# Optimization experiments

Measured on AMD Instinct MI355X. Metric: run time of the kernel, lower is better.

The kernel has to match this reference:

```python
import jax, jax.numpy as jnp
import numpy as np

G = 8          # groups
PATCH = 4      # encoder patch conv kernel/stride
MD = 4         # correlation max displacement -> (2*MD+1)^2 = 81 neighbours
BNEPS = 1e-5
LNEPS = 1e-5

# finite-difference gradient kernel (assumed: forward differences on a C-grid)
GRAD_K = jnp.array([[[[0., 0., 0.], [0., -1., 1.], [0., 0., 0.]]],
                    [[[0., 0., 0.], [0., -1., 0.], [0., 1., 0.]]]], dtype=jnp.float32)

def _vort_kernel():
    # assumed 6x6 Biot-Savart-like vorticity->velocity kernel (CalculusOperators not in source)
    c = 2.5
    ys, xs = np.mgrid[0:6, 0:6].astype(np.float32)
    r2 = (ys - c) ** 2 + (xs - c) ** 2
    u = -(ys - c) / (2.0 * np.pi * r2)
    v = (xs - c) / (2.0 * np.pi * r2)
    return jnp.asarray(np.stack([u, v])[:, None])  # [2,1,6,6]
VORT_K = _vort_kernel()

def conv2d(x, w, pad, stride=1):
    return jax.lax.conv_general_dilated(x, w, (stride, stride), [(pad, pad), (pad, pad)],
                                        dimension_numbers=('NCHW', 'OIHW', 'NCHW'))

def bn(x, g, b):
    # inference-mode BatchNorm with running_mean=0, running_var=1
    return x * (g / jnp.sqrt(1.0 + BNEPS))[None, :, None, None] + b[None, :, None, None]

def up2x(x):
    def lerp_axis(x, axis):
        n = x.shape[axis]
        c = jnp.arange(2 * n, dtype=x.dtype) * (n - 1) / (2 * n - 1)
        i0 = jnp.floor(c).astype(jnp.int32)
        i1 = jnp.minimum(i0 + 1, n - 1)
        w = c - i0.astype(x.dtype)
        a0 = jnp.take(x, i0, axis=axis)
        a1 = jnp.take(x, i1, axis=axis)
        shp = [1] * x.ndim; shp[axis] = 2 * n
        w = w.reshape(shp)
        return a0 * (1 - w) + a1 * w
    return lerp_axis(lerp_axis(x, 2), 3)

def double_conv_up(x, w1, g1, b1, w2, g2, b2):
    x = jax.nn.relu(bn(conv2d(up2x(x), w1, 1), g1, b1))
    return jax.nn.relu(bn(conv2d(up2x(x), w2, 1), g2, b2))

@jax.checkpoint
def correlation(f1, f2):
    # PWC-Net style FunctionCorrelation: mean over channels of f1 * shifted f2, 81 shifts
    N, C, H, W = f1.shape
    f2p = jnp.pad(f2, ((0, 0), (0, 0), (MD, MD), (MD, MD)))
    outs = [jnp.mean(f1 * f2p[:, :, dy:dy + H, dx:dx + W], axis=1)
            for dy in range(2 * MD + 1) for dx in range(2 * MD + 1)]
    return jnp.stack(outs, axis=1)  # [N, 81, H, W]

def cgrid_to_motion(u, v, shape):
    mu = (u[:, :, 1:-1, 1:] + u[:, :, 1:-1, :-1]) * 0.5
    mv = (v[:, :, 1:, 1:-1] + v[:, :, :-1, 1:-1]) * 0.5
    m = jnp.concatenate([mu, mv], axis=1)
    h, w = shape
    up = (m.shape[2] - h) // 2
    left = (m.shape[3] - w) // 2
    return m[:, :, up:up + h, left:left + w]

def calc_phi_velocity(phi, shape):
    vel = conv2d(phi, GRAD_K, 1)
    return cgrid_to_motion(vel[:, 0:1, :, :-1], vel[:, 1:2, :-1, :], shape)

def calc_vort_velocity(stream, shape):
    s = stream[:, :, :-1, :-1]
    vel = conv2d(s, VORT_K, 5)  # full-padding conv == conv_transpose of flipped kernel
    return cgrid_to_motion(vel[:, 0:1, 2:-2, 2:-3], vel[:, 1:2, 2:-3, 2:-2], shape)

def bilinear_sample(f, px, py):
    # f [N,C,H,W]; px,py [N,H,W] absolute coords, border clamp
    H, W = f.shape[-2], f.shape[-1]
    px = jnp.clip(px, 0.0, W - 1.0)
    py = jnp.clip(py, 0.0, H - 1.0)
    x0 = jnp.floor(px); y0 = jnp.floor(py)
    wx = (px - x0)[:, None]; wy = (py - y0)[:, None]
    x0i = x0.astype(jnp.int32); y0i = y0.astype(jnp.int32)
    x1i = jnp.minimum(x0i + 1, W - 1); y1i = jnp.minimum(y0i + 1, H - 1)
    gat = jax.vmap(lambda fi, yi, xi: fi[:, yi, xi])
    v00 = gat(f, y0i, x0i); v01 = gat(f, y0i, x1i)
    v10 = gat(f, y1i, x0i); v11 = gat(f, y1i, x1i)
    return (v00 * (1 - wx) + v01 * wx) * (1 - wy) + (v10 * (1 - wx) + v11 * wx) * wy

def warp(f, vel, sign):
    N, _, H, W = f.shape
    ys, xs = jnp.meshgrid(jnp.arange(H, dtype=f.dtype), jnp.arange(W, dtype=f.dtype), indexing='ij')
    return bilinear_sample(f, xs[None] - sign * vel[:, 0], ys[None] - sign * vel[:, 1])

def bfecc_warp(f, vel):
    f1 = warp(f, vel, 1.0)
    fb = warp(f1, vel, -1.0)
    return warp(f + 0.5 * (f - fb), vel, 1.0)

def _forward(prev, next, texture, mask, boundary,
             enc_w, enc_b,
             phi_w1, phi_g1, phi_b1, phi_w2, phi_g2, phi_b2, phi_ow, phi_ob,
             vor_w1, vor_g1, vor_b1, vor_w2, vor_g2, vor_b2, vor_ow, vor_ob,
             phi_weight, vorticity_weight,
             ln_g, ln_b, fc1_w, fc1_b, fc2_w, fc2_b):
    B, C, H, W = prev.shape
    shape = texture.shape[-2:]
    pm = (prev * mask[:, None]).reshape(B * G, C // G, H, W)
    pb = (prev * boundary[:, None]).reshape(B * G, C // G, H, W)
    nm = (next * mask[:, None]).reshape(B * G, C // G, H, W)
    enc = lambda x: conv2d(x, enc_w, 0, PATCH) + enc_b[None, :, None, None]
    f_nm = enc(nm)
    corr = jnp.concatenate([correlation(enc(pm), f_nm), correlation(enc(pb), f_nm)], axis=1)
    phi = (conv2d(double_conv_up(corr, phi_w1, phi_g1, phi_b1, phi_w2, phi_g2, phi_b2), phi_ow, 0)
           + phi_ob[None, :, None, None]) * phi_weight
    vort = (conv2d(double_conv_up(corr, vor_w1, vor_g1, vor_b1, vor_w2, vor_g2, vor_b2), vor_ow, 0)
            + vor_ob[None, :, None, None]) * vorticity_weight * H
    helm = jnp.concatenate([phi, vort], axis=1)  # [B*G, 2, H, W]
    vel_phi = calc_phi_velocity(helm[:, 0:1], shape)
    vel_vort = calc_vort_velocity(helm[:, 1:2], shape)
    vel = vel_phi + vel_vort
    Bt, Ct, Ht, Wt = texture.shape
    tex = texture.reshape(B * G, Ct // G, Ht, Wt)
    pred = bfecc_warp(tex, vel).reshape(B, Ct, Ht, Wt)
    xp = jnp.transpose(pred, (0, 2, 3, 1))  # [B,H,W,C]
    mu = jnp.mean(xp, -1, keepdims=True)
    var = jnp.var(xp, -1, keepdims=True)
    y = (xp - mu) / jnp.sqrt(var + LNEPS) * ln_g + ln_b
    y = jax.nn.gelu(y @ fc1_w.T + fc1_b, approximate=False)
    y = y @ fc2_w.T + fc2_b
    return pred + jnp.transpose(y, (0, 3, 1, 2))

def setup_inputs():
    ks = jax.random.split(jax.random.key(0), 20)
    B, C, H, W = 4, 64, 260, 260
    Ht, Wt = 258, 258
    D = 128           # correlation_dim
    cg = C // G       # 8 channels per group
    ed = 8            # encoder_dim // groups = 64 // 8
    n = lambda i, shp, s=1.0: jax.random.normal(ks[i], shp, jnp.float32) * s
    return {
        'prev': n(0, (B, C, H, W)), 'next': n(1, (B, C, H, W)),
        'texture': n(2, (B, C, Ht, Wt)),
        'mask': jax.random.uniform(ks[3], (B, H, W), jnp.float32),
        'boundary': jax.random.uniform(ks[4], (B, H, W), jnp.float32),
        'enc_w': n(5, (D, cg, PATCH, PATCH), 0.05), 'enc_b': n(6, (D,), 0.02),
        'phi_w1': n(7, (ed, 162, 3, 3), 0.05), 'phi_g1': jnp.ones(ed), 'phi_b1': jnp.zeros(ed),
        'phi_w2': n(8, (ed, ed, 3, 3), 0.05), 'phi_g2': jnp.ones(ed), 'phi_b2': jnp.zeros(ed),
        'phi_ow': n(9, (1, ed, 1, 1), 0.05), 'phi_ob': n(10, (1,), 0.02),
        'vor_w1': n(11, (ed, 162, 3, 3), 0.05), 'vor_g1': jnp.ones(ed), 'vor_b1': jnp.zeros(ed),
        'vor_w2': n(12, (ed, ed, 3, 3), 0.05), 'vor_g2': jnp.ones(ed), 'vor_b2': jnp.zeros(ed),
        'vor_ow': n(13, (1, ed, 1, 1), 0.05), 'vor_ob': n(14, (1,), 0.02),
        'phi_weight': jnp.array([0.5], jnp.float32),
        'vorticity_weight': jnp.array([0.005], jnp.float32),
        'ln_g': jnp.ones(C), 'ln_b': jnp.zeros(C),
        'fc1_w': n(15, (C, C), 0.05), 'fc1_b': n(16, (C,), 0.02),
        'fc2_w': n(17, (C, C), 0.05), 'fc2_b': n(18, (C,), 0.02),
    }

def reference(prev, next, texture, mask, boundary,
              enc_w, enc_b,
              phi_w1, phi_g1, phi_b1, phi_w2, phi_g2, phi_b2, phi_ow, phi_ob,
              vor_w1, vor_g1, vor_b1, vor_w2, vor_g2, vor_b2, vor_ow, vor_ob,
              phi_weight, vorticity_weight,
              ln_g, ln_b, fc1_w, fc1_b, fc2_w, fc2_b):
    return _forward(prev, next, texture, mask, boundary,
                    enc_w, enc_b,
                    phi_w1, phi_g1, phi_b1, phi_w2, phi_g2, phi_b2, phi_ow, phi_ob,
                    vor_w1, vor_g1, vor_b1, vor_w2, vor_g2, vor_b2, vor_ow, vor_ob,
                    phi_weight, vorticity_weight,
                    ln_g, ln_b, fc1_w, fc1_b, fc2_w, fc2_b)
```

## Files before the change

kernel.cpp:

```cpp
#include <hip/hip_runtime.h>
#include <math.h>


#define NIMG 32
#define HW 260
#define HWT 258
#define EG 65
#define EGP (EG*EG)
#define DENC 128
#define PIX_T (HWT*HWT)
#define PIX_H (HW*HW)

__global__ void k_wt(const float* __restrict__ w, float* __restrict__ wt) {
    int e = blockIdx.x * 256 + threadIdx.x;
    if (e < 128 * 128) {
        int d = e >> 7, i = e & 127;
        wt[i * 128 + d] = w[e];
    }
}

__global__ __launch_bounds__(128) void k_enc(
    const float* __restrict__ src,
    const float* __restrict__ mul,
    const float* __restrict__ wt,
    const float* __restrict__ bias,
    float* __restrict__ out)
{
    int xt = blockIdx.x;
    int yo = blockIdx.y;
    int n  = blockIdx.z;
    int bi = n >> 3, g = n & 7;
    int xo0 = xt * 16;
    __shared__ __align__(16) float patch[2048];
    int tid = threadIdx.x;
    const float* sbase = src + (size_t)(bi * 64 + g * 8) * PIX_H;
    const float* mbase = mul + (size_t)bi * PIX_H;
    int row0 = yo * 4, col0 = xo0 * 4;
    for (int e = tid; e < 2048; e += 128) {
        int c = e >> 8, r = (e >> 6) & 3, col = e & 63;
        int gc = col0 + col;
        float v = 0.f;
        if (gc < HW) {
            int off = (row0 + r) * HW + gc;
            v = sbase[(size_t)c * PIX_H + off] * mbase[off];
        }
        patch[e] = v;
    }
    __syncthreads();
    int d = tid;
    float acc[16];
    float bv = bias[d];
#pragma unroll
    for (int p = 0; p < 16; ++p) acc[p] = bv;
    const float4* p4 = (const float4*)patch;
    for (int j = 0; j < 32; ++j) {
        float w0 = wt[(j * 4 + 0) * 128 + d];
        float w1 = wt[(j * 4 + 1) * 128 + d];
        float w2 = wt[(j * 4 + 2) * 128 + d];
        float w3 = wt[(j * 4 + 3) * 128 + d];
#pragma unroll
        for (int p = 0; p < 16; ++p) {
            float4 v = p4[j * 16 + p];
            acc[p] += w0 * v.x + w1 * v.y + w2 * v.z + w3 * v.w;
        }
    }
    size_t ob = ((size_t)(n * EG + yo) * EG + xo0) * 128 + d;
#pragma unroll
    for (int p = 0; p < 16; ++p)
        if (xo0 + p < EG) out[ob + (size_t)p * 128] = acc[p];
}

__global__ __launch_bounds__(128) void k_corr(
    const float* __restrict__ f1,
    const float* __restrict__ f2,
    float* __restrict__ corr,
    int obase)
{
    int bx = blockIdx.x;
    int dy = bx >> 1, xt = bx & 1;
    int y  = blockIdx.y;
    int n  = blockIdx.z;
    int xs = xt ? 33 : 0;
    int nx = xt ? 32 : 33;
    __shared__ __align__(16) float s1[33 * 132];
    __shared__ __align__(16) float s2[41 * 132];
    int tid = threadIdx.x;
    const float4* g1 = (const float4*)(f1 + ((size_t)(n * EG + y) * EG + xs) * 128);
    float4* s1v = (float4*)s1;
    for (int e = tid; e < nx * 32; e += 128) {
        int xl = e >> 5, c4 = e & 31;
        s1v[xl * 33 + c4] = g1[xl * 32 + c4];
    }
    int y2 = y + dy - 4;
    bool yok = (y2 >= 0 && y2 < EG);
    const float4* g2 = (const float4*)(f2 + (yok ? ((size_t)(n * EG + y2) * EG) * 128 : 0));
    float4* s2v = (float4*)s2;
    for (int e = tid; e < 41 * 32; e += 128) {
        int xl = e >> 5, c4 = e & 31;
        int xg = xs - 4 + xl;
        float4 v = make_float4(0.f, 0.f, 0.f, 0.f);
        if (yok && xg >= 0 && xg < EG) v = g2[xg * 32 + c4];
        s2v[xl * 33 + c4] = v;
    }
    __syncthreads();
    int nact = nx * 3;
    if (tid < nact) {
        int q, xl;
        if (xt) { q = tid >> 5; xl = tid & 31; }
        else    { q = tid / 33; xl = tid - q * 33; }
        int dx0 = q * 3;
        float4 a0 = make_float4(0,0,0,0), a1 = a0, a2 = a0;
        const float4* r1 = (const float4*)s1 + xl * 33;
        const float4* r2 = (const float4*)s2 + (xl + dx0) * 33;
#pragma unroll 8
        for (int i = 0; i < 32; ++i) {
            float4 a = r1[i];
            float4 b0 = r2[i], b1 = r2[33 + i], b2 = r2[66 + i];
            a0.x += a.x * b0.x; a0.y += a.y * b0.y; a0.z += a.z * b0.z; a0.w += a.w * b0.w;
            a1.x += a.x * b1.x; a1.y += a.y * b1.y; a1.z += a.z * b1.z; a1.w += a.w * b1.w;
            a2.x += a.x * b2.x; a2.y += a.y * b2.y; a2.z += a.z * b2.z; a2.w += a.w * b2.w;
        }
        float s[3];
        s[0] = (a0.x + a0.y + a0.z + a0.w) * (1.0f / 128.0f);
        s[1] = (a1.x + a1.y + a1.z + a1.w) * (1.0f / 128.0f);
        s[2] = (a2.x + a2.y + a2.z + a2.w) * (1.0f / 128.0f);
#pragma unroll
        for (int m = 0; m < 3; ++m) {
            int o = obase + dy * 9 + dx0 + m;
            corr[(size_t)(n * 162 + o) * EGP + y * EG + xs + xl] = s[m];
        }
    }
}

__global__ __launch_bounds__(256) void k_conv1(
    const float* __restrict__ corr,
    const float* __restrict__ w_phi,
    const float* __restrict__ w_vor,
    const float* __restrict__ g_phi, const float* __restrict__ b_phi,
    const float* __restrict__ g_vor, const float* __restrict__ b_vor,
    float* __restrict__ h1)
{
    int yp = blockIdx.x;
    int n  = blockIdx.y;
    int y0 = yp * 4;
    __shared__ float upc[6 * 6 * 132];
    __shared__ float wch[16 * 6 * 9];
    __shared__ float s_xw[132];
    __shared__ int   s_xi0[132];
    __shared__ int   s_xi1[132];
    __shared__ float s_yw[6];
    __shared__ int   s_yj0[6];
    __shared__ int   s_yj1[6];
    __shared__ int   s_yv[6];
    int tid = threadIdx.x;
    if (tid < 132) {
        int xu = tid - 1;
        if (xu >= 0 && xu <= 129) {
            float cx = (float)(xu * 64) / 129.0f;
            int i0 = (int)cx;
            int i1 = i0 + 1; if (i1 > 64) i1 = 64;
            s_xw[tid] = cx - (float)i0;
            s_xi0[tid] = i0;
            s_xi1[tid] = i1;
        } else { s_xi0[tid] = -1; s_xi1[tid] = 0; s_xw[tid] = 0.f; }
    }
    if (tid >= 132 && tid < 138) {
        int r = tid - 132;
        int yy = y0 - 1 + r;
        if (yy >= 0 && yy <= 129) {
            float cy = (float)(yy * 64) / 129.0f;
            int i0 = (int)cy;
            int i1 = i0 + 1; if (i1 > 64) i1 = 64;
            s_yw[r] = cy - (float)i0;
            s_yj0[r] = i0;
            s_yj1[r] = i1;
            s_yv[r] = 1;
        } else { s_yw[r] = 0.f; s_yj0[r] = 0; s_yj1[r] = 0; s_yv[r] = 0; }
    }
    int og = tid / 26, xg = tid - og * 26;
    int x0 = xg * 5;
    bool act = (og < 8);
    float acc[2][4][5] = {};
    for (int cc = 0; cc < 27; ++cc) {
        int cb = cc * 6;
        __syncthreads();
        for (int e = tid; e < 4752; e += 256) {
            int r = e / 792, rem = e - r * 792, ci = rem / 132, xx = rem - ci * 132;
            float val = 0.f;
            int xi0 = s_xi0[xx];
            if (s_yv[r] && xi0 >= 0) {
                const float* cp = corr + (size_t)(n * 162 + cb + ci) * EGP;
                int J0 = s_yj0[r] * 65, J1 = s_yj1[r] * 65;
                int xi1 = s_xi1[xx];
                float wxv = s_xw[xx];
                float a0 = __ldg(cp + J0 + xi0), a1 = __ldg(cp + J0 + xi1);
                float b0 = __ldg(cp + J1 + xi0), b1 = __ldg(cp + J1 + xi1);
                float tp = a0 + wxv * (a1 - a0);
                float bt = b0 + wxv * (b1 - b0);
                val = tp + s_yw[r] * (bt - tp);
            }
            upc[e] = val;
        }
        for (int e = tid; e < 864; e += 256) {
            int oc = e / 54, rem = e - oc * 54, ci = rem / 9, k = rem - ci * 9;
            int t2 = oc >> 3, o = oc & 7;
            wch[e] = (t2 ? w_vor : w_phi)[(o * 162 + cb + ci) * 9 + k];
        }
        __syncthreads();
        if (act) {
            for (int ci = 0; ci < 6; ++ci) {
                float wr[2][9];
#pragma unroll
                for (int p = 0; p < 2; ++p)
#pragma unroll
                    for (int k = 0; k < 9; ++k)
                        wr[p][k] = wch[((og + 8 * p) * 6 + ci) * 9 + k];
#pragma unroll
                for (int r = 0; r < 6; ++r) {
                    float u7[7];
                    const float* up = &upc[(r * 6 + ci) * 132 + x0];
#pragma unroll
                    for (int m = 0; m < 7; ++m) u7[m] = up[m];
#pragma unroll
                    for (int ky = 0; ky < 3; ++ky) {
                        int yi = r - ky;
                        if (yi < 0 || yi > 3) continue;
#pragma unroll
                        for (int p = 0; p < 2; ++p)
#pragma unroll
                            for (int kx = 0; kx < 3; ++kx) {
                                float w = wr[p][ky * 3 + kx];
#pragma unroll
                                for (int xi = 0; xi < 5; ++xi)
                                    acc[p][yi][xi] += w * u7[xi + kx];
                            }
                    }
                }
            }
        }
    }
    if (act) {
        const float bnsc = 1.0f / sqrtf(1.0f + 1e-5f);
#pragma unroll
        for (int p = 0; p < 2; ++p) {
            float gsc = (p ? g_vor[og] : g_phi[og]) * bnsc;
            float bia = (p ? b_vor[og] : b_phi[og]);
            size_t pb = (size_t)((p * 32 + n) * 8 + og) * 16900;
#pragma unroll
            for (int yi = 0; yi < 4; ++yi) {
                int row = y0 + yi;
                if (row < 130) {
#pragma unroll
                    for (int xi = 0; xi < 5; ++xi) {
                        float v = acc[p][yi][xi] * gsc + bia;
                        h1[pb + (size_t)row * 130 + (x0 + xi)] = fmaxf(v, 0.f);
                    }
                }
            }
        }
    }
}

__global__ __launch_bounds__(256) void k_conv2(
    const float* __restrict__ h1,
    const float* __restrict__ w_phi2, const float* __restrict__ w_vor2,
    const float* __restrict__ g_phi2, const float* __restrict__ b_phi2,
    const float* __restrict__ g_vor2, const float* __restrict__ b_vor2,
    const float* __restrict__ ow_phi, const float* __restrict__ ob_phi,
    const float* __restrict__ ow_vor, const float* __restrict__ ob_vor,
    const float* __restrict__ phi_weight, const float* __restrict__ vort_weight,
    float* __restrict__ helm)
{
    int y = blockIdx.x, n = blockIdx.y;
    __shared__ float hraw[8320];
    __shared__ float wch[1152];
    __shared__ float bns[16], bnb[16], owv[16], obv[2], wm[2];
    int tid = threadIdx.x;
    int ylo = y - 1; if (ylo < 0) ylo = 0;
    int R0 = (int)((float)(ylo * 129) / 259.0f);
    for (int e = tid; e < 8320; e += 256) {
        int t2 = e / 4160, rem = e - t2 * 4160;
        int j = rem / 1040, rem2 = rem - j * 1040;
        int ci = rem2 / 130, xx = rem2 - ci * 130;
        int R = R0 + j; if (R > 129) R = 129;
        hraw[e] = h1[(size_t)((t2 * 32 + n) * 8 + ci) * 16900 + R * 130 + xx];
    }
    for (int e = tid; e < 1152; e += 256) {
        int t2 = e / 576, rem = e - t2 * 576;
        int o = rem / 72, rem2 = rem - o * 72;
        int ci = rem2 / 9, k = rem2 - ci * 9;
        wch[e] = (t2 ? w_vor2 : w_phi2)[(o * 8 + ci) * 9 + k];
    }
    if (tid < 16) {
        int t2 = tid >> 3, o = tid & 7;
        bns[tid] = (t2 ? g_vor2[o] : g_phi2[o]) * (1.0f / sqrtf(1.0f + 1e-5f));
        bnb[tid] = (t2 ? b_vor2[o] : b_phi2[o]);
        owv[tid] = (t2 ? ow_vor[o] : ow_phi[o]);
    }
    if (tid == 0) {
        obv[0] = ob_phi[0]; obv[1] = ob_vor[0];
        wm[0] = phi_weight[0]; wm[1] = vort_weight[0] * 260.0f;
    }
    __syncthreads();
    for (int x = tid; x < HW; x += 256) {
        float wy[3]; int rj0[3], rj1[3]; bool vy[3];
#pragma unroll
        for (int ky = 0; ky < 3; ++ky) {
            int yy = y - 1 + ky;
            vy[ky] = (yy >= 0 && yy < HW);
            if (vy[ky]) {
                float cy = (float)(yy * 129) / 259.0f;
                int i0 = (int)cy; wy[ky] = cy - (float)i0;
                int i1 = i0 + 1; if (i1 > 129) i1 = 129;
                rj0[ky] = i0 - R0; rj1[ky] = i1 - R0;
            } else { wy[ky] = 0; rj0[ky] = 0; rj1[ky] = 0; }
        }
        float wxv[3]; int c0[3], c1[3]; bool vx[3];
#pragma unroll
        for (int kx = 0; kx < 3; ++kx) {
            int xxp = x - 1 + kx;
            vx[kx] = (xxp >= 0 && xxp < HW);
            if (vx[kx]) {
                float cx = (float)(xxp * 129) / 259.0f;
                int i0 = (int)cx; wxv[kx] = cx - (float)i0;
                int i1 = i0 + 1; if (i1 > 129) i1 = 129;
                c0[kx] = i0; c1[kx] = i1;
            } else { wxv[kx] = 0; c0[kx] = 0; c1[kx] = 0; }
        }
        float res[2];
#pragma unroll
        for (int t2 = 0; t2 < 2; ++t2) {
            float acc[8] = {0,0,0,0,0,0,0,0};
            for (int ci = 0; ci < 8; ++ci) {
#pragma unroll
                for (int ky = 0; ky < 3; ++ky) {
                    if (!vy[ky]) continue;
                    const float* r0p = &hraw[((t2 * 4 + rj0[ky]) * 8 + ci) * 130];
                    const float* r1p = &hraw[((t2 * 4 + rj1[ky]) * 8 + ci) * 130];
                    float u3[3];
#pragma unroll
                    for (int kx = 0; kx < 3; ++kx) {
                        if (vx[kx]) {
                            float tp = r0p[c0[kx]] + wxv[kx] * (r0p[c1[kx]] - r0p[c0[kx]]);
                            float bt = r1p[c0[kx]] + wxv[kx] * (r1p[c1[kx]] - r1p[c0[kx]]);
                            u3[kx] = tp + wy[ky] * (bt - tp);
                        } else u3[kx] = 0.f;
                    }
#pragma unroll
                    for (int o = 0; o < 8; ++o) {
                        const float* wp = &wch[((t2 * 8 + o) * 8 + ci) * 9 + ky * 3];
                        acc[o] += wp[0] * u3[0] + wp[1] * u3[1] + wp[2] * u3[2];
                    }
                }
            }
            float dot = 0.f;
#pragma unroll
            for (int o = 0; o < 8; ++o) {
                float hv = fmaxf(acc[o] * bns[t2 * 8 + o] + bnb[t2 * 8 + o], 0.f);
                dot += owv[t2 * 8 + o] * hv;
            }
            res[t2] = (dot + obv[t2]) * wm[t2];
        }
        helm[(size_t)(n * 2 + 0) * PIX_H + y * HW + x] = res[0];
        helm[(size_t)(n * 2 + 1) * PIX_H + y * HW + x] = res[1];
    }
}

__device__ __forceinline__ float K0f(int a, int b) {
    if (a < 0 || a > 5 || b < 0 || b > 5) return 0.f;
    float fa = (float)a - 2.5f, fb = (float)b - 2.5f;
    float r2 = fa * fa + fb * fb;
    return -fa / (6.28318530717958647692f * r2);
}
__device__ __forceinline__ float K1f(int a, int b) {
    if (a < 0 || a > 5 || b < 0 || b > 5) return 0.f;
    float fa = (float)a - 2.5f, fb = (float)b - 2.5f;
    float r2 = fa * fa + fb * fb;
    return fb / (6.28318530717958647692f * r2);
}

__global__ __launch_bounds__(256) void k_vel(
    const float* __restrict__ helm, float* __restrict__ vel)
{
    int idx = blockIdx.x * 256 + threadIdx.x;
    if (idx >= NIMG * PIX_T) return;
    int n = idx / PIX_T, pix = idx - n * PIX_T;
    int yy = pix / HWT, xx = pix - yy * HWT;
    const float* phi = helm + (size_t)(n * 2) * PIX_H;
    const float* s   = helm + (size_t)(n * 2 + 1) * PIX_H;
    float sv[7][7];
#pragma unroll
    for (int di = 0; di < 7; ++di) {
        int i = yy + di - 3;
#pragma unroll
        for (int dj = 0; dj < 7; ++dj) {
            int j = xx + dj - 3;
            sv[di][dj] = (i >= 0 && i < 259 && j >= 0 && j < 259) ? s[i * HW + j] : 0.f;
        }
    }
    float ax = 0.5f * (phi[(yy + 1) * HW + xx + 2] - phi[(yy + 1) * HW + xx]);
#pragma unroll
    for (int a = 0; a < 6; ++a)
#pragma unroll
        for (int d = 0; d < 7; ++d) {
            float coef = K0f(a, d) + K0f(a, d - 1);
            ax += 0.5f * coef * sv[a + 1][d];
        }
    float ay = 0.5f * (phi[(yy + 2) * HW + xx + 1] - phi[yy * HW + xx + 1]);
#pragma unroll
    for (int d = 0; d < 7; ++d)
#pragma unroll
        for (int b = 0; b < 6; ++b) {
            float coef = K1f(d, b) + K1f(d - 1, b);
            ay += 0.5f * coef * sv[d][b + 1];
        }
    vel[(size_t)(n * 2) * PIX_T + pix]     = ax;
    vel[(size_t)(n * 2 + 1) * PIX_T + pix] = ay;
}

__device__ __forceinline__ float bsample(const float* __restrict__ plane,
                                         float px, float py) {
    px = fminf(fmaxf(px, 0.f), 257.f);
    py = fminf(fmaxf(py, 0.f), 257.f);
    float fx = floorf(px), fy = floorf(py);
    int x0 = (int)fx, y0 = (int)fy;
    float wx = px - fx, wy = py - fy;
    int x1 = x0 + 1; if (x1 > 257) x1 = 257;
    int y1 = y0 + 1; if (y1 > 257) y1 = 257;
    const float* r0 = plane + y0 * HWT;
    const float* r1 = plane + y1 * HWT;
    float v00 = r0[x0], v01 = r0[x1], v10 = r1[x0], v11 = r1[x1];
    float tp = v00 + wx * (v01 - v00);
    float bt = v10 + wx * (v11 - v10);
    return tp + wy * (bt - tp);
}

__global__ __launch_bounds__(256) void k_warp(
    const float* __restrict__ src,
    const float* __restrict__ vel,
    float sign,
    const float* __restrict__ tex,
    int mode,
    float* __restrict__ out)
{
    int idx = blockIdx.x * 256 + threadIdx.x;
    if (idx >= NIMG * 8 * PIX_T) return;
    int plane_i = idx / PIX_T;
    int pix = idx - plane_i * PIX_T;
    int n = plane_i >> 3;
    int y = pix / HWT, x = pix - y * HWT;
    float vx = vel[(size_t)(n * 2) * PIX_T + pix];
    float vy = vel[(size_t)(n * 2 + 1) * PIX_T + pix];
    const float* plane = src + (size_t)plane_i * PIX_T;
    float v = bsample(plane, (float)x - sign * vx, (float)y - sign * vy);
    if (mode) v = 1.5f * tex[idx] - 0.5f * v;
    out[idx] = v;
}

__global__ __launch_bounds__(256, 2) void k_lnmlp(
    float* __restrict__ out,
    const float* __restrict__ lng, const float* __restrict__ lnb,
    const float* __restrict__ w1, const float* __restrict__ b1,
    const float* __restrict__ w2, const float* __restrict__ b2)
{
    int yy = blockIdx.x, b = blockIdx.y;
    __shared__ __align__(16) float sw1[4096];
    __shared__ __align__(16) float sw2t[4096];
    __shared__ float sb1[64], sb2[64], sg[64], sbt[64];
    int tid = threadIdx.x;
    for (int e = tid; e < 4096; e += 256) {
        sw1[e] = w1[e];
        sw2t[(e & 63) * 64 + (e >> 6)] = w2[e];
    }
    if (tid < 64) { sb1[tid] = b1[tid]; sb2[tid] = b2[tid]; sg[tid] = lng[tid]; sbt[tid] = lnb[tid]; }
    __syncthreads();
    float* base = out + (size_t)b * 64 * PIX_T + (size_t)yy * HWT;
    for (int x = tid; x < HWT; x += 256) {
        float sum = 0.f, sumsq = 0.f;
        for (int k = 0; k < 64; ++k) {
            float v = base[(size_t)k * PIX_T + x];
            sum += v; sumsq += v * v;
        }
        float mu = sum * (1.0f / 64.0f);
        float var = sumsq * (1.0f / 64.0f) - mu * mu;
        float inv = 1.0f / sqrtf(var + 1e-5f);
        float xn[64];
#pragma unroll
        for (int k = 0; k < 64; ++k) {
            float v = base[(size_t)k * PIX_T + x];
            xn[k] = (v - mu) * inv * sg[k] + sbt[k];
        }
        float acc2[64];
#pragma unroll
        for (int j2 = 0; j2 < 64; ++j2) acc2[j2] = 0.f;
        for (int j = 0; j < 64; ++j) {
            float t = sb1[j];
            const float4* wrow = (const float4*)&sw1[j * 64];
#pragma unroll
            for (int k4 = 0; k4 < 16; ++k4) {
                float4 w = wrow[k4];
                t += xn[4 * k4] * w.x + xn[4 * k4 + 1] * w.y
                   + xn[4 * k4 + 2] * w.z + xn[4 * k4 + 3] * w.w;
            }
            float hj = 0.5f * t * (1.0f + erff(t * 0.70710678118654752f));
            const float4* w2row = (const float4*)&sw2t[j * 64];
#pragma unroll
            for (int q = 0; q < 16; ++q) {
                float4 w = w2row[q];
                acc2[4 * q]     += hj * w.x;
                acc2[4 * q + 1] += hj * w.y;
                acc2[4 * q + 2] += hj * w.z;
                acc2[4 * q + 3] += hj * w.w;
            }
        }
#pragma unroll
        for (int j2 = 0; j2 < 64; ++j2)
            base[(size_t)j2 * PIX_T + x] += sb2[j2] + acc2[j2];
    }
}

extern "C" void kernel_launch(void* const* d_in, const int* in_sizes, int n_in,
                              void* d_out, int out_size, void* d_ws, size_t ws_size,
                              hipStream_t stream) {
    const float* prev       = (const float*)d_in[0];
    const float* next       = (const float*)d_in[1];
    const float* texture    = (const float*)d_in[2];
    const float* mask       = (const float*)d_in[3];
    const float* boundary   = (const float*)d_in[4];
    const float* enc_w      = (const float*)d_in[5];
    const float* enc_b      = (const float*)d_in[6];
    const float* phi_w1     = (const float*)d_in[7];
    const float* phi_g1     = (const float*)d_in[8];
    const float* phi_b1     = (const float*)d_in[9];
    const float* phi_w2     = (const float*)d_in[10];
    const float* phi_g2     = (const float*)d_in[11];
    const float* phi_b2     = (const float*)d_in[12];
    const float* phi_ow     = (const float*)d_in[13];
    const float* phi_ob     = (const float*)d_in[14];
    const float* vor_w1     = (const float*)d_in[15];
    const float* vor_g1     = (const float*)d_in[16];
    const float* vor_b1     = (const float*)d_in[17];
    const float* vor_w2     = (const float*)d_in[18];
    const float* vor_g2     = (const float*)d_in[19];
    const float* vor_b2     = (const float*)d_in[20];
    const float* vor_ow     = (const float*)d_in[21];
    const float* vor_ob     = (const float*)d_in[22];
    const float* phi_weight = (const float*)d_in[23];
    const float* vor_weight = (const float*)d_in[24];
    const float* ln_g       = (const float*)d_in[25];
    const float* ln_b       = (const float*)d_in[26];
    const float* fc1_w      = (const float*)d_in[27];
    const float* fc1_b      = (const float*)d_in[28];
    const float* fc2_w      = (const float*)d_in[29];
    const float* fc2_b      = (const float*)d_in[30];

    float* ws = (float*)d_ws;
    float* F_NM = ws + 0;
    float* F_A  = ws + 17305600;
    float* CORR = ws + 34611200;
    float* WT   = ws + 56513600;
    float* H1   = ws + 0;
    float* HELM = ws + 17305600;
    float* VEL  = ws + 21632000;
    float* F1B  = ws + 34611200;
    float* F2B  = ws + 0;
    float* OUT  = (float*)d_out;

    k_wt<<<dim3(64), dim3(256), 0, stream>>>(enc_w, WT);

    dim3 encg(5, 65, 32);
    k_enc<<<encg, dim3(128), 0, stream>>>(next, mask, WT, enc_b, F_NM);
    k_enc<<<encg, dim3(128), 0, stream>>>(prev, mask, WT, enc_b, F_A);

    dim3 corrg(18, 65, 32);
    k_corr<<<corrg, dim3(128), 0, stream>>>(F_A, F_NM, CORR, 0);
    k_enc<<<encg, dim3(128), 0, stream>>>(prev, boundary, WT, enc_b, F_A);
    k_corr<<<corrg, dim3(128), 0, stream>>>(F_A, F_NM, CORR, 81);

    k_conv1<<<dim3(33, 32), dim3(256), 0, stream>>>(
        CORR, phi_w1, vor_w1, phi_g1, phi_b1, vor_g1, vor_b1, H1);

    k_conv2<<<dim3(260, 32), dim3(256), 0, stream>>>(
        H1, phi_w2, vor_w2, phi_g2, phi_b2, vor_g2, vor_b2,
        phi_ow, phi_ob, vor_ow, vor_ob, phi_weight, vor_weight, HELM);

    int nv = NIMG * PIX_T;
    k_vel<<<dim3((nv + 255) / 256), dim3(256), 0, stream>>>(HELM, VEL);

    int nw = NIMG * 8 * PIX_T;
    int wb = (nw + 255) / 256;
    k_warp<<<dim3(wb), dim3(256), 0, stream>>>(texture, VEL,  1.0f, texture, 0, F1B);
    k_warp<<<dim3(wb), dim3(256), 0, stream>>>(F1B,     VEL, -1.0f, texture, 1, F2B);
    k_warp<<<dim3(wb), dim3(256), 0, stream>>>(F2B,     VEL,  1.0f, texture, 0, OUT);

    k_lnmlp<<<dim3(258, 4), dim3(256), 0, stream>>>(
        OUT, ln_g, ln_b, fc1_w, fc1_b, fc2_w, fc2_b);
}
```

Baseline: 3.075 ms.

## Split conv1 input channels across grid z with a reduction kernel; halve corr LDS

The first upsample-conv stage now splits its 27 input-channel chunks into three slices along grid z. Each slice writes raw partial sums to a workspace buffer, and a new elementwise kernel sums the three partials and applies BN and ReLU. This triples the block count for a grid that was small relative to the GPU, at the cost of extra partial-sum traffic and one more launch. Separately, the correlation kernel stages channels in two 64-channel halves using float4 shared arrays. This roughly halves its LDS footprint so more blocks can be resident, but adds barriers.

```diff
diff --git a/kernel.cpp b/kernel.cpp
--- a/kernel.cpp
+++ b/kernel.cpp
@@ -7,9 +7,9 @@
 #define HWT 258
 #define EG 65
 #define EGP (EG*EG)
-#define DENC 128
 #define PIX_T (HWT*HWT)
 #define PIX_H (HW*HW)
+#define H1N 8652800
 
 __global__ void k_wt(const float* __restrict__ w, float* __restrict__ wt) {
     int e = blockIdx.x * 256 + threadIdx.x;
@@ -82,44 +82,48 @@
     int n  = blockIdx.z;
     int xs = xt ? 33 : 0;
     int nx = xt ? 32 : 33;
-    __shared__ __align__(16) float s1[33 * 132];
-    __shared__ __align__(16) float s2[41 * 132];
+    __shared__ __align__(16) float4 s1[33 * 17];
+    __shared__ __align__(16) float4 s2[41 * 17];
     int tid = threadIdx.x;
     const float4* g1 = (const float4*)(f1 + ((size_t)(n * EG + y) * EG + xs) * 128);
-    float4* s1v = (float4*)s1;
-    for (int e = tid; e < nx * 32; e += 128) {
-        int xl = e >> 5, c4 = e & 31;
-        s1v[xl * 33 + c4] = g1[xl * 32 + c4];
-    }
     int y2 = y + dy - 4;
     bool yok = (y2 >= 0 && y2 < EG);
     const float4* g2 = (const float4*)(f2 + (yok ? ((size_t)(n * EG + y2) * EG) * 128 : 0));
-    float4* s2v = (float4*)s2;
-    for (int e = tid; e < 41 * 32; e += 128) {
-        int xl = e >> 5, c4 = e & 31;
-        int xg = xs - 4 + xl;
-        float4 v = make_float4(0.f, 0.f, 0.f, 0.f);
-        if (yok && xg >= 0 && xg < EG) v = g2[xg * 32 + c4];
-        s2v[xl * 33 + c4] = v;
-    }
-    __syncthreads();
-    int nact = nx * 3;
-    if (tid < nact) {
-        int q, xl;
-        if (xt) { q = tid >> 5; xl = tid & 31; }
-        else    { q = tid / 33; xl = tid - q * 33; }
-        int dx0 = q * 3;
-        float4 a0 = make_float4(0,0,0,0), a1 = a0, a2 = a0;
-        const float4* r1 = (const float4*)s1 + xl * 33;
-        const float4* r2 = (const float4*)s2 + (xl + dx0) * 33;
+    int q, xl;
+    if (xt) { q = tid >> 5; xl = tid & 31; }
+    else    { q = tid / 33; xl = tid - q * 33; }
+    int dx0 = q * 3;
+    bool act = tid < nx * 3;
+    float4 a0 = make_float4(0,0,0,0), a1 = a0, a2 = a0;
+    for (int half = 0; half < 2; ++half) {
+        int cb = half * 16;
+        __syncthreads();
+        for (int e = tid; e < nx * 16; e += 128) {
+            int r = e >> 4, c4 = e & 15;
+            s1[r * 17 + c4] = g1[r * 32 + cb + c4];
+        }
+        for (int e = tid; e < 41 * 16; e += 128) {
+            int r = e >> 4, c4 = e & 15;
+            int xg = xs - 4 + r;
+            float4 v = make_float4(0.f, 0.f, 0.f, 0.f);
+            if (yok && xg >= 0 && xg < EG) v = g2[xg * 32 + cb + c4];
+            s2[r * 17 + c4] = v;
+        }
+        __syncthreads();
+        if (act) {
+            const float4* r1 = s1 + xl * 17;
+            const float4* r2 = s2 + (xl + dx0) * 17;
 #pragma unroll 8
-        for (int i = 0; i < 32; ++i) {
-            float4 a = r1[i];
-            float4 b0 = r2[i], b1 = r2[33 + i], b2 = r2[66 + i];
-            a0.x += a.x * b0.x; a0.y += a.y * b0.y; a0.z += a.z * b0.z; a0.w += a.w * b0.w;
-            a1.x += a.x * b1.x; a1.y += a.y * b1.y; a1.z += a.z * b1.z; a1.w += a.w * b1.w;
-            a2.x += a.x * b2.x; a2.y += a.y * b2.y; a2.z += a.z * b2.z; a2.w += a.w * b2.w;
-        }
+            for (int i = 0; i < 16; ++i) {
+                float4 a = r1[i];
+                float4 b0 = r2[i], b1 = r2[17 + i], b2 = r2[34 + i];
+                a0.x += a.x * b0.x; a0.y += a.y * b0.y; a0.z += a.z * b0.z; a0.w += a.w * b0.w;
+                a1.x += a.x * b1.x; a1.y += a.y * b1.y; a1.z += a.z * b1.z; a1.w += a.w * b1.w;
+                a2.x += a.x * b2.x; a2.y += a.y * b2.y; a2.z += a.z * b2.z; a2.w += a.w * b2.w;
+            }
+        }
+    }
+    if (act) {
         float s[3];
         s[0] = (a0.x + a0.y + a0.z + a0.w) * (1.0f / 128.0f);
         s[1] = (a1.x + a1.y + a1.z + a1.w) * (1.0f / 128.0f);
@@ -136,12 +140,11 @@
     const float* __restrict__ corr,
     const float* __restrict__ w_phi,
     const float* __restrict__ w_vor,
-    const float* __restrict__ g_phi, const float* __restrict__ b_phi,
-    const float* __restrict__ g_vor, const float* __restrict__ b_vor,
-    float* __restrict__ h1)
+    float* __restrict__ part)
 {
     int yp = blockIdx.x;
     int n  = blockIdx.y;
+    int zp = blockIdx.z;
     int y0 = yp * 4;
     __shared__ float upc[6 * 6 * 132];
     __shared__ float wch[16 * 6 * 9];
@@ -181,7 +184,7 @@
     int x0 = xg * 5;
     bool act = (og < 8);
     float acc[2][4][5] = {};
-    for (int cc = 0; cc < 27; ++cc) {
+    for (int cc = zp * 9; cc < zp * 9 + 9; ++cc) {
         int cb = cc * 6;
         __syncthreads();
         for (int e = tid; e < 4752; e += 256) {
@@ -240,25 +243,47 @@
         }
     }
     if (act) {
-        const float bnsc = 1.0f / sqrtf(1.0f + 1e-5f);
+        float* pbuf = part + (size_t)zp * H1N;
 #pragma unroll
         for (int p = 0; p < 2; ++p) {
-            float gsc = (p ? g_vor[og] : g_phi[og]) * bnsc;
-            float bia = (p ? b_vor[og] : b_phi[og]);
             size_t pb = (size_t)((p * 32 + n) * 8 + og) * 16900;
 #pragma unroll
             for (int yi = 0; yi < 4; ++yi) {
                 int row = y0 + yi;
                 if (row < 130) {
 #pragma unroll
-                    for (int xi = 0; xi < 5; ++xi) {
-                        float v = acc[p][yi][xi] * gsc + bia;
-                        h1[pb + (size_t)row * 130 + (x0 + xi)] = fmaxf(v, 0.f);
-                    }
+                    for (int xi = 0; xi < 5; ++xi)
+                        pbuf[pb + (size_t)row * 130 + (x0 + xi)] = acc[p][yi][xi];
                 }
             }
         }
     }
+}
+
+__global__ __launch_bounds__(256) void k_h1red(
+    const float* __restrict__ part,
+    const float* __restrict__ g_phi, const float* __restrict__ b_phi,
+    const float* __restrict__ g_vor, const float* __restrict__ b_vor,
+    float* __restrict__ h1)
+{
+    int i4 = blockIdx.x * 256 + threadIdx.x;
+    if (i4 >= H1N / 4) return;
+    size_t i = (size_t)i4 * 4;
+    int c2 = (int)(i / 16900);
+    int o = c2 & 7, t2 = c2 >> 8;
+    const float bnsc = 1.0f / sqrtf(1.0f + 1e-5f);
+    float gsc = (t2 ? g_vor[o] : g_phi[o]) * bnsc;
+    float bia = (t2 ? b_vor[o] : b_phi[o]);
+    const float4* p0 = (const float4*)(part);
+    const float4* p1 = (const float4*)(part + H1N);
+    const float4* p2 = (const float4*)(part + 2 * (size_t)H1N);
+    float4 a = p0[i4], b = p1[i4], c = p2[i4];
+    float4 r;
+    r.x = fmaxf((a.x + b.x + c.x) * gsc + bia, 0.f);
+    r.y = fmaxf((a.y + b.y + c.y) * gsc + bia, 0.f);
+    r.z = fmaxf((a.z + b.z + c.z) * gsc + bia, 0.f);
+    r.w = fmaxf((a.w + b.w + c.w) * gsc + bia, 0.f);
+    ((float4*)h1)[i4] = r;
 }
 
 __global__ __launch_bounds__(256) void k_conv2(
@@ -559,7 +584,8 @@
     float* F_A  = ws + 17305600;
     float* CORR = ws + 34611200;
     float* WT   = ws + 56513600;
-    float* H1   = ws + 0;
+    float* PART = ws + 0;
+    float* H1   = ws + 25958400;
     float* HELM = ws + 17305600;
     float* VEL  = ws + 21632000;
     float* F1B  = ws + 34611200;
@@ -577,8 +603,10 @@
     k_enc<<<encg, dim3(128), 0, stream>>>(prev, boundary, WT, enc_b, F_A);
     k_corr<<<corrg, dim3(128), 0, stream>>>(F_A, F_NM, CORR, 81);
 
-    k_conv1<<<dim3(33, 32), dim3(256), 0, stream>>>(
-        CORR, phi_w1, vor_w1, phi_g1, phi_b1, vor_g1, vor_b1, H1);
+    k_conv1<<<dim3(33, 32, 3), dim3(256), 0, stream>>>(
+        CORR, phi_w1, vor_w1, PART);
+    k_h1red<<<dim3((H1N / 4 + 255) / 256), dim3(256), 0, stream>>>(
+        PART, phi_g1, phi_b1, vor_g1, vor_b1, H1);
 
     k_conv2<<<dim3(260, 32), dim3(256), 0, stream>>>(
         H1, phi_w2, vor_w2, phi_g2, phi_b2, vor_g2, vor_b2,
```

Measured after the change: 2.839 ms. -7.7%, faster.
